# Kernel optimization log

Measured on AMD Instinct MI355X. Metric: run time of the kernel, lower is better.

## Reference

```python
import jax, jax.numpy as jnp
from jax import lax
import numpy as np
import math

B, N, A = 4096, 8, 5
IN_CH, HW = 3, 5
POS = 2
OBS_IN = POS + N            # 10
OBS_ACT_IN = OBS_IN + A     # 15
D = 128                     # obs_output_dim == d_k == embed width
STATE_DIM = 32 + OBS_IN     # 42
SAP_IN = 32 + OBS_ACT_IN    # 47


def setup_inputs() -> dict:
    key = jax.random.key(0)
    ks = jax.random.split(key, 24)
    w = lambda k, shape: (jax.random.normal(k, shape) * 0.05).astype(jnp.float32)
    return {
        "agent_states": jax.random.normal(ks[0], (B, N, IN_CH, HW, HW), jnp.float32),
        "agent_global_positions": jax.random.normal(ks[1], (B, N, POS), jnp.float32),
        "agent_one_hot_encoding": jax.random.uniform(ks[2], (B, N, N), jnp.float32),
        "policies": jax.random.uniform(ks[3], (B, N, A), jnp.float32),
        "actions": jax.random.uniform(ks[4], (B, N, A), jnp.float32),
        "conv1_w": w(ks[5], (16, IN_CH, 3, 3)), "conv1_b": w(ks[6], (16,)),
        "conv2_w": w(ks[7], (32, 16, 3, 3)),    "conv2_b": w(ks[8], (32,)),
        "se_w": w(ks[9], (STATE_DIM, 128)),     "se_b": w(ks[10], (128,)),
        "key_w": w(ks[11], (128, D)),           "key_b": w(ks[12], (D,)),
        "query_w": w(ks[13], (128, D)),         "query_b": w(ks[14], (D,)),
        "sap_w": w(ks[15], (SAP_IN, 128)),      "sap_b": w(ks[16], (128,)),
        "av_w": w(ks[17], (128, 128)),          "av_b": w(ks[18], (128,)),
        "f1_w": w(ks[19], (128, 64)),           "f1_b": w(ks[20], (64,)),
        "f2_w": w(ks[21], (64, 1)),             "f2_b": w(ks[22], (1,)),
    }


def _conv(x, w, b):
    y = lax.conv_general_dilated(x, w, (1, 1), 'VALID',
                                 dimension_numbers=('NCHW', 'OIHW', 'NCHW'))
    return y + b[None, :, None, None]


def reference(agent_states, agent_global_positions, agent_one_hot_encoding,
              policies, actions,
              conv1_w, conv1_b, conv2_w, conv2_b,
              se_w, se_b, key_w, key_b, query_w, query_b,
              sap_w, sap_b, av_w, av_b, f1_w, f1_b, f2_w, f2_b):
    leaky = lambda x: jnp.where(x >= 0, x, 0.01 * x)
    b, n = agent_states.shape[0], agent_states.shape[1]

    # CNN encoder: [B*N,3,5,5] -> [B*N,32,1,1]
    x = agent_states.reshape(b * n, IN_CH, HW, HW)
    h = leaky(_conv(x, conv1_w, conv1_b))
    h = leaky(_conv(h, conv2_w, conv2_b))
    pose_id = jnp.concatenate([agent_global_positions, agent_one_hot_encoding], axis=-1)
    states = jnp.concatenate([h.reshape(b, n, -1), pose_id], axis=-1)  # [B,N,42]

    states_embed = jnp.tanh(states @ se_w + se_b)                      # [B,N,128]
    k = states_embed @ key_w + key_b
    q = states_embed @ query_w + query_b
    weight = jax.nn.softmax(jnp.einsum('bqd,bkd->bqk', q, k) / math.sqrt(D), axis=-1)

    obs_actions = jnp.concatenate([states, actions], axis=-1)          # [B,N,47]
    obs_policy = jnp.concatenate([states, policies], axis=-1)         # [B,N,47]
    # place_policies puts the policy vector on the diagonal (i==j), action elsewhere.
    eye = jnp.eye(n, dtype=states.dtype)[None, :, :, None]             # [1,N,N,1]
    oap = eye * obs_policy[:, None, :, :] + (1.0 - eye) * obs_actions[:, None, :, :]  # [B,i,j,47]

    oap_embed = jnp.tanh(oap @ sap_w + sap_b)                          # [B,N,N,128]
    attn_vals = jnp.tanh(oap_embed @ av_w + av_b)                      # [B,i,j,128]

    # node_features[b,a,i,d] = sum_j weight[b,a,j] * attn_vals[b,i,j,d]
    # (replaces the original repeat -> broadcast-multiply -> sum over O(N^4) tensor)
    node_features = jnp.einsum('baj,bijd->baid', weight, attn_vals)    # [B,N,N,128]

    v = jnp.tanh(node_features @ f1_w + f1_b)
    value = v @ f2_w + f2_b                                            # [B,N,N,1]
    return value, weight
```

## Files before the change

### kernel.cpp

```cpp
#include <hip/hip_runtime.h>
#include <math.h>

#define NB 4096
#define NA 8
#define BN (NB*NA)

#define OFF_SE   0
#define OFF_SAP  4096
#define OFF_AV   8192
#define OFF_F1   16384
#define OFF_M    20480
#define OFF_U    28672
#define OFF_W2P  28800

typedef short short8 __attribute__((ext_vector_type(8)));
typedef float f32x4 __attribute__((ext_vector_type(4)));

#define MFMA(a,b,c) __builtin_amdgcn_mfma_f32_16x16x32_bf16(a,b,c,0,0,0)

__device__ __forceinline__ float fast_tanh(float x){
    float e = __expf(2.0f*x);
    return 1.0f - 2.0f*__builtin_amdgcn_rcpf(e+1.0f);
}
__device__ __forceinline__ unsigned bfr(float x){
    unsigned u = __float_as_uint(x);
    return (u + 0x7fffu + ((u>>16)&1u)) >> 16;
}
__device__ __forceinline__ unsigned pk2(float lo, float hi){
    return bfr(lo) | (bfr(hi)<<16);
}
__device__ __forceinline__ float bf2f(unsigned short s){
    return __uint_as_float(((unsigned)s)<<16);
}
__device__ __forceinline__ short8 fragld(const unsigned* p){
    union { uint4 u; short8 s; } cv;
    cv.u = *(const uint4*)p;
    return cv.s;
}

__global__ __launch_bounds__(256) void kW(const float* __restrict__ se_w,
        const float* __restrict__ sap_w, const float* __restrict__ av_w,
        const float* __restrict__ f1_w, const float* __restrict__ qw,
        const float* __restrict__ kw, const float* __restrict__ qb,
        const float* __restrict__ w2,
        unsigned* __restrict__ ws){
    int idx = blockIdx.x*256 + threadIdx.x;
    if (idx < 4096){
        int w = idx, tile = w>>9, rem = w&511;
        int ft = rem>>6, r2 = (rem>>2)&15, wi = rem&3;
        int f2 = tile*16 + r2, f1 = ft*8 + wi*2;
        float lo = (f1   < 42)? se_w[f1*128+f2]     : 0.f;
        float hi = (f1+1 < 42)? se_w[(f1+1)*128+f2] : 0.f;
        ws[OFF_SE + w] = pk2(lo,hi);
    } else if (idx < 8192){
        int w = idx-4096, tile = w>>9, rem = w&511;
        int ft = rem>>6, r2 = (rem>>2)&15, wi = rem&3;
        int f2 = tile*16 + r2, f1 = ft*8 + wi*2;
        float lo = (f1   < 47)? sap_w[f1*128+f2]     : 0.f;
        float hi = (f1+1 < 47)? sap_w[(f1+1)*128+f2] : 0.f;
        ws[OFF_SAP + w] = pk2(lo,hi);
    } else if (idx < 16384){
        int w = idx-8192, tile = w>>10, rem = w&1023;
        int ft = rem>>6, r2 = (rem>>2)&15, wi = rem&3;
        int f2 = tile*16 + r2, f1 = ft*8 + wi*2;
        ws[OFF_AV + w] = pk2(av_w[f1*128+f2], av_w[(f1+1)*128+f2]);
    } else if (idx < 20480){
        int w = idx-16384, tile = w>>10, rem = w&1023;
        int ft = rem>>6, r2 = (rem>>2)&15, wi = rem&3;
        int f2 = tile*16 + r2, f1 = ft*8 + wi*2;
        ws[OFF_F1 + w] = pk2(f1_w[f1*64+f2], f1_w[(f1+1)*64+f2]);
    } else if (idx < 28672){
        int w = idx-20480, tile = w>>10, rem = w&1023;
        int ft = rem>>6, r2 = (rem>>2)&15, wi = rem&3;
        int f2 = tile*16 + r2, e0 = ft*8 + wi*2;
        float lo=0.f, hi=0.f;
        for (int d=0; d<128; ++d){
            float kv = kw[f2*128+d];
            lo += qw[e0*128+d]*kv;
            hi += qw[(e0+1)*128+d]*kv;
        }
        ws[OFF_M + w] = pk2(lo,hi);
    } else if (idx < 28800){
        int f = idx-28672;
        float a = 0.f;
        for (int d=0; d<128; ++d) a += qb[d]*kw[f*128+d];
        ((float*)ws)[OFF_U + f] = a;
    } else if (idx < 31360){
        int w = idx-28800;
        int ftile = w/1280, rem = w - ftile*1280;
        int ft = rem>>6, r2 = (rem>>2)&15, wi = rem&3;
        int f = ftile*16 + r2, k0 = ft*8 + wi*2;
        float lo = (k0   < 144)? w2[f*144+k0]   : 0.f;
        float hi = (k0+1 < 144)? w2[f*144+k0+1] : 0.f;
        ws[OFF_W2P + w] = pk2(lo,hi);
    }
}

__global__ __launch_bounds__(256,2) void kF(const unsigned* __restrict__ ws,
        const float* __restrict__ xin, const float* __restrict__ pos,
        const float* __restrict__ oneh, const float* __restrict__ acts,
        const float* __restrict__ pols,
        const float* __restrict__ w1, const float* __restrict__ b1,
        const float* __restrict__ b2,
        const float* __restrict__ se_b,
        const float* __restrict__ sap_b, const float* __restrict__ av_b,
        const float* __restrict__ f1_b, const float* __restrict__ f2_w,
        const float* __restrict__ f2_b,
        float* __restrict__ wout, float* __restrict__ value){
    __shared__ unsigned SM[9216];
    __shared__ unsigned stPk[4096];
    __shared__ unsigned sA64[2304];
    __shared__ unsigned sP64[2304];
    __shared__ float s_w[512];
    __shared__ float s_bias[384];
    __shared__ float s_ub[256];
    const int t = threadIdx.x;
    const int wv = t>>6, lane = t&63;
    const int g = lane>>4, c = lane&15;

    float* c_in   = (float*)SM;
    unsigned* hpk = SM + 1216;
    float* c_ap   = (float*)(SM+6336);
    float* c_pose = (float*)(SM+6496);
    float* c_w1   = (float*)(SM+6656);
    float* c_b1   = (float*)(SM+7088);
    float* c_b2   = (float*)(SM+7104);
    for (int q=t; q<432; q+=256) c_w1[q] = w1[q];
    if (t<16) c_b1[t] = b1[t];
    if (t<32) c_b2[t] = b2[t];
    for (int q=t; q<512; q+=256) hpk[(q>>7)*1280 + 1152 + (q&127)] = 0;
    for (int q=t; q<384; q+=256)
        s_bias[q] = (q<128)? sap_b[q] : (q<256)? av_b[q-128] : (q<320)? f1_b[q-256] : f2_w[q-320];
    s_ub[t] = (t<128)? ((const float*)ws)[OFF_U+t] : se_b[t-128];

    for (int p=0; p<4; ++p){
        const size_t a0g = (size_t)blockIdx.x*64 + p*16;
        for (int q=t; q<1200; q+=256){
            int ag=q/75, r=q-ag*75;
            c_in[ag*76+r] = xin[a0g*75+q];
        }
        for (int q=t; q<160; q+=256){
            int ag=q/10, k=q-ag*10;
            c_ap[q]   = (k<5)? acts[(a0g+ag)*5+k] : pols[(a0g+ag)*5+(k-5)];
            c_pose[q] = (k<2)? pos[(a0g+ag)*2+k]  : oneh[(a0g+ag)*8+(k-2)];
        }
        __syncthreads();
        {
            const int ag = t&15, oc = t>>4;
            float w[27];
            #pragma unroll
            for (int i=0;i<27;++i) w[i]=c_w1[oc*27+i];
            float out[9];
            float bb = c_b1[oc];
            #pragma unroll
            for (int q=0;q<9;++q) out[q]=bb;
            #pragma unroll
            for (int ic=0;ic<3;++ic){
                float pin[25];
                #pragma unroll
                for (int i=0;i<25;++i) pin[i]=c_in[ag*76+ic*25+i];
                #pragma unroll
                for (int y=0;y<3;++y)
                  #pragma unroll
                  for (int x=0;x<3;++x)
                    #pragma unroll
                    for (int ky=0;ky<3;++ky)
                      #pragma unroll
                      for (int kx=0;kx<3;++kx)
                        out[y*3+x] += pin[(y+ky)*5+(x+kx)] * w[ic*9+ky*3+kx];
            }
            unsigned short* hp16 = (unsigned short*)(hpk + p*1280);
            #pragma unroll
            for (int q=0;q<9;++q){
                float v = out[q];
                v = (v>=0.f)? v : 0.01f*v;
                int k = oc*9+q;
                int word = (k>>3)*64 + ag*4 + ((k>>1)&3);
                hp16[word*2 + (k&1)] = (unsigned short)bfr(v);
            }
        }
        {
            const int ft4 = t>>6, r = (t>>2)&15, wi = t&3;
            const int f0 = 32 + ft4*8 + wi*2;
            float a0=0.f,a1=0.f,p0=0.f,p1=0.f;
            if (f0 < 42){ a0 = c_pose[r*10 + f0-32]; p0 = a0; }
            else if (f0 < 47){ a0 = c_ap[r*10 + f0-42]; p0 = c_ap[r*10+5 + f0-42]; }
            if (f0+1 < 42){ a1 = c_pose[r*10 + f0-31]; p1 = a1; }
            else if (f0+1 < 47){ a1 = c_ap[r*10 + f0-41]; p1 = c_ap[r*10+5 + f0-41]; }
            int word = p*512 + (4+ft4)*64 + r*4 + wi;
            stPk[word]      = pk2(a0,a1);
            stPk[2048+word] = pk2(p0,p1);
        }
        __syncthreads();
    }
    {
        const unsigned* hw = hpk + wv*1280;
        f32x4 c2[2];
        c2[0] = (f32x4){0.f,0.f,0.f,0.f};
        c2[1] = (f32x4){0.f,0.f,0.f,0.f};
        #pragma unroll
        for (int kt=0; kt<5; ++kt){
            short8 hb  = fragld(hw + kt*256 + lane*4);
            short8 w0f = fragld(ws + OFF_W2P + kt*256 + lane*4);
            short8 w1f = fragld(ws + OFF_W2P + 1280 + kt*256 + lane*4);
            c2[0] = MFMA(w0f, hb, c2[0]);
            c2[1] = MFMA(w1f, hb, c2[1]);
        }
        #pragma unroll
        for (int ft=0; ft<2; ++ft){
            const float* bp = &c_b2[ft*16 + g*4];
            float d0 = c2[ft][0]+bp[0]; d0 = (d0>=0.f)? d0 : 0.01f*d0;
            float d1 = c2[ft][1]+bp[1]; d1 = (d1>=0.f)? d1 : 0.01f*d1;
            float d2 = c2[ft][2]+bp[2]; d2 = (d2>=0.f)? d2 : 0.01f*d2;
            float d3 = c2[ft][3]+bp[3]; d3 = (d3>=0.f)? d3 : 0.01f*d3;
            int word = wv*512 + (2*ft + (g>>1))*64 + c*4 + (g&1)*2;
            uint2 pw = make_uint2(pk2(d0,d1), pk2(d2,d3));
            *(uint2*)&stPk[word] = pw;
            *(uint2*)&stPk[2048+word] = pw;
        }
    }
    __syncthreads();

    const int tile = blockIdx.x*4 + wv;
    short8 bfA0 = fragld(&stPk[wv*512 + lane*4]);
    short8 bfA1 = fragld(&stPk[wv*512 + 256 + lane*4]);
    short8 bfP0 = fragld(&stPk[2048 + wv*512 + lane*4]);
    short8 bfP1 = fragld(&stPk[2048 + wv*512 + 256 + lane*4]);
    unsigned (*s_stage)[2048] = (unsigned (*)[2048])&SM[0];
    unsigned* U1 = &SM[4096];
    unsigned* wS = &U1[wv*1280];
    unsigned* tS = &U1[wv*1280 + 1024];

    uint4 r0, r1;
#define PREF(off) { r0 = *(const uint4*)(ws + (off) + t*4); \
                    r1 = *(const uint4*)(ws + (off) + 1024 + t*4); }
#define WR(b) { *(uint4*)&s_stage[b][t*4] = r0; *(uint4*)&s_stage[b][1024 + t*4] = r1; }

    PREF(OFF_SE); WR(0);
    __syncthreads();

    f32x4 acc[8];
    #pragma unroll
    for (int i=0;i<8;++i) acc[i] = (f32x4){0.f,0.f,0.f,0.f};
    PREF(OFF_SE + 2048);
    #pragma unroll
    for (int ft=0; ft<4; ++ft){
        short8 a0 = fragld(&s_stage[0][ft*512 + lane*4]);
        short8 a1 = fragld(&s_stage[0][ft*512 + 256 + lane*4]);
        acc[ft] = MFMA(a0, bfA0, acc[ft]);
        acc[ft] = MFMA(a1, bfA1, acc[ft]);
    }
    WR(1); __syncthreads();
    PREF(OFF_M);
    #pragma unroll
    for (int ft=4; ft<8; ++ft){
        short8 a0 = fragld(&s_stage[1][(ft-4)*512 + lane*4]);
        short8 a1 = fragld(&s_stage[1][(ft-4)*512 + 256 + lane*4]);
        acc[ft] = MFMA(a0, bfA0, acc[ft]);
        acc[ft] = MFMA(a1, bfA1, acc[ft]);
    }
    WR(0);
    #pragma unroll
    for (int ft=0; ft<8; ++ft){
        const float* bp = &s_ub[128 + ft*16 + g*4];
        float d0 = fast_tanh(acc[ft][0]+bp[0]);
        float d1 = fast_tanh(acc[ft][1]+bp[1]);
        float d2 = fast_tanh(acc[ft][2]+bp[2]);
        float d3 = fast_tanh(acc[ft][3]+bp[3]);
        int word = (2*ft + (g>>1))*64 + c*4 + (g&1)*2;
        *(uint2*)&wS[word] = make_uint2(pk2(d0,d1), pk2(d2,d3));
    }
    short8 ef[4];
    #pragma unroll
    for (int kt=0; kt<4; ++kt) ef[kt] = fragld(&wS[kt*256 + lane*4]);
    __syncthreads();

    f32x4 L = (f32x4){0.f,0.f,0.f,0.f};
    #pragma unroll
    for (int i=0; i<4; ++i){
        const int nextOff = (i<3)? (OFF_M + (i+1)*2048) : OFF_SAP;
        PREF(nextOff);
        f32x4 a2[2];
        a2[0] = (f32x4){0.f,0.f,0.f,0.f};
        a2[1] = (f32x4){0.f,0.f,0.f,0.f};
        #pragma unroll
        for (int ftl=0; ftl<2; ++ftl)
          #pragma unroll
          for (int kt=0; kt<4; ++kt){
            short8 mf = fragld(&s_stage[i&1][ftl*1024 + kt*256 + lane*4]);
            a2[ftl] = MFMA(mf, ef[kt], a2[ftl]);
          }
        WR((i+1)&1);
        #pragma unroll
        for (int ftl=0; ftl<2; ++ftl){
            const float* up = &s_ub[(2*i+ftl)*16 + g*4];
            int word = (2*ftl + (g>>1))*64 + c*4 + (g&1)*2;
            *(uint2*)&tS[word] = make_uint2(pk2(a2[ftl][0]+up[0], a2[ftl][1]+up[1]),
                                            pk2(a2[ftl][2]+up[2], a2[ftl][3]+up[3]));
        }
        short8 tf = fragld(&tS[lane*4]);
        L = MFMA(tf, ef[i], L);
        __syncthreads();
    }
    {
        float sc[4];
        #pragma unroll
        for (int q=0;q<4;++q) sc[q] = L[q]*0.08838834764831845f;
        #pragma unroll
        for (int q=0;q<4;++q){
            float m = sc[q];
            m = fmaxf(m, __shfl_xor(m,1));
            m = fmaxf(m, __shfl_xor(m,2));
            m = fmaxf(m, __shfl_xor(m,4));
            float ex = __expf(sc[q]-m);
            float su = ex;
            su += __shfl_xor(su,1);
            su += __shfl_xor(su,2);
            su += __shfl_xor(su,4);
            sc[q] = ex/su;
        }
        if ((c>>3) == (g>>1)){
            int lb = wv*2 + (g>>1);
            int batch = tile*2 + (g>>1);
            int idx = ((g&1)*4)*8 + (c&7);
            #pragma unroll
            for (int q=0;q<4;++q){
                float v = sc[q];
                wout[batch*64 + idx + q*8] = v;
                s_w[lb*64 + idx + q*8] = v;
            }
        }
    }

    f32x4 aS[2][8];
    #pragma unroll
    for (int v=0;v<2;++v)
      #pragma unroll
      for (int i=0;i<8;++i) aS[v][i] = (f32x4){0.f,0.f,0.f,0.f};
    PREF(OFF_SAP + 2048);
    #pragma unroll
    for (int ft=0; ft<4; ++ft){
        short8 a0 = fragld(&s_stage[0][ft*512 + lane*4]);
        short8 a1 = fragld(&s_stage[0][ft*512 + 256 + lane*4]);
        aS[0][ft] = MFMA(a0, bfA0, aS[0][ft]);
        aS[0][ft] = MFMA(a1, bfA1, aS[0][ft]);
        aS[1][ft] = MFMA(a0, bfP0, aS[1][ft]);
        aS[1][ft] = MFMA(a1, bfP1, aS[1][ft]);
    }
    WR(1); __syncthreads();
    PREF(OFF_AV);
    #pragma unroll
    for (int ft=4; ft<8; ++ft){
        short8 a0 = fragld(&s_stage[1][(ft-4)*512 + lane*4]);
        short8 a1 = fragld(&s_stage[1][(ft-4)*512 + 256 + lane*4]);
        aS[0][ft] = MFMA(a0, bfA0, aS[0][ft]);
        aS[0][ft] = MFMA(a1, bfA1, aS[0][ft]);
        aS[1][ft] = MFMA(a0, bfP0, aS[1][ft]);
        aS[1][ft] = MFMA(a1, bfP1, aS[1][ft]);
    }
    WR(0);
    short8 spA[4], spP[4];
    #pragma unroll
    for (int ft=0; ft<8; ++ft){
        const float* bp = &s_bias[ft*16 + g*4];
        float d0 = fast_tanh(aS[0][ft][0]+bp[0]);
        float d1 = fast_tanh(aS[0][ft][1]+bp[1]);
        float d2 = fast_tanh(aS[0][ft][2]+bp[2]);
        float d3 = fast_tanh(aS[0][ft][3]+bp[3]);
        int word = (2*ft + (g>>1))*64 + c*4 + (g&1)*2;
        *(uint2*)&wS[word] = make_uint2(pk2(d0,d1), pk2(d2,d3));
    }
    #pragma unroll
    for (int kt=0; kt<4; ++kt) spA[kt] = fragld(&wS[kt*256 + lane*4]);
    #pragma unroll
    for (int ft=0; ft<8; ++ft){
        const float* bp = &s_bias[ft*16 + g*4];
        float d0 = fast_tanh(aS[1][ft][0]+bp[0]);
        float d1 = fast_tanh(aS[1][ft][1]+bp[1]);
        float d2 = fast_tanh(aS[1][ft][2]+bp[2]);
        float d3 = fast_tanh(aS[1][ft][3]+bp[3]);
        int word = (2*ft + (g>>1))*64 + c*4 + (g&1)*2;
        *(uint2*)&wS[word] = make_uint2(pk2(d0,d1), pk2(d2,d3));
    }
    #pragma unroll
    for (int kt=0; kt<4; ++kt) spP[kt] = fragld(&wS[kt*256 + lane*4]);
    __syncthreads();

    f32x4 aV[2][8];
    #pragma unroll
    for (int v=0;v<2;++v)
      #pragma unroll
      for (int i=0;i<8;++i) aV[v][i] = (f32x4){0.f,0.f,0.f,0.f};
    short8 avA[4], avP[4];
    #pragma unroll
    for (int i=0; i<4; ++i){
        const int nextOff = (i<3)? (OFF_AV + (i+1)*2048) : OFF_F1;
        PREF(nextOff);
        #pragma unroll
        for (int ftl=0; ftl<2; ++ftl){
            const int ft = 2*i + ftl;
            #pragma unroll
            for (int kt=0; kt<4; ++kt){
                short8 af = fragld(&s_stage[i&1][ftl*1024 + kt*256 + lane*4]);
                aV[0][ft] = MFMA(af, spA[kt], aV[0][ft]);
                aV[1][ft] = MFMA(af, spP[kt], aV[1][ft]);
            }
        }
        WR((i+1)&1);
        if (i==3){
            #pragma unroll
            for (int ft=0; ft<8; ++ft){
                const float* bp = &s_bias[128 + ft*16 + g*4];
                float d0 = fast_tanh(aV[0][ft][0]+bp[0]);
                float d1 = fast_tanh(aV[0][ft][1]+bp[1]);
                float d2 = fast_tanh(aV[0][ft][2]+bp[2]);
                float d3 = fast_tanh(aV[0][ft][3]+bp[3]);
                int word = (2*ft + (g>>1))*64 + c*4 + (g&1)*2;
                *(uint2*)&wS[word] = make_uint2(pk2(d0,d1), pk2(d2,d3));
            }
            #pragma unroll
            for (int kt=0; kt<4; ++kt) avA[kt] = fragld(&wS[kt*256 + lane*4]);
            #pragma unroll
            for (int ft=0; ft<8; ++ft){
                const float* bp = &s_bias[128 + ft*16 + g*4];
                float d0 = fast_tanh(aV[1][ft][0]+bp[0]);
                float d1 = fast_tanh(aV[1][ft][1]+bp[1]);
                float d2 = fast_tanh(aV[1][ft][2]+bp[2]);
                float d3 = fast_tanh(aV[1][ft][3]+bp[3]);
                int word = (2*ft + (g>>1))*64 + c*4 + (g&1)*2;
                *(uint2*)&wS[word] = make_uint2(pk2(d0,d1), pk2(d2,d3));
            }
            #pragma unroll
            for (int kt=0; kt<4; ++kt) avP[kt] = fragld(&wS[kt*256 + lane*4]);
        }
        __syncthreads();
    }

    f32x4 aF[2][4];
    #pragma unroll
    for (int v=0;v<2;++v)
      #pragma unroll
      for (int i=0;i<4;++i) aF[v][i] = (f32x4){0.f,0.f,0.f,0.f};
    PREF(OFF_F1 + 2048);
    #pragma unroll
    for (int ftl=0; ftl<2; ++ftl)
      #pragma unroll
      for (int kt=0; kt<4; ++kt){
        short8 af = fragld(&s_stage[0][ftl*1024 + kt*256 + lane*4]);
        aF[0][ftl] = MFMA(af, avA[kt], aF[0][ftl]);
        aF[1][ftl] = MFMA(af, avP[kt], aF[1][ftl]);
      }
    WR(1); __syncthreads();
    #pragma unroll
    for (int ftl=0; ftl<2; ++ftl)
      #pragma unroll
      for (int kt=0; kt<4; ++kt){
        short8 af = fragld(&s_stage[1][ftl*1024 + kt*256 + lane*4]);
        aF[0][2+ftl] = MFMA(af, avA[kt], aF[0][2+ftl]);
        aF[1][2+ftl] = MFMA(af, avP[kt], aF[1][2+ftl]);
      }
    {
        int row = wv*16 + c;
        #pragma unroll
        for (int v=0;v<2;++v){
            unsigned* dst = v? sP64 : sA64;
            #pragma unroll
            for (int ft=0; ft<4; ++ft){
                int idx = row*36 + ft*8 + 2*g;
                *(uint2*)&dst[idx] = make_uint2(pk2(aF[v][ft][0], aF[v][ft][1]),
                                                pk2(aF[v][ft][2], aF[v][ft][3]));
            }
        }
    }
    __syncthreads();
    float* s_b64 = (float*)U1;
    {
        const int bqa = t>>2, ccg = t&3;
        const int bq = bqa>>3, a = bqa&7;
        const float* wp = &s_w[bq*64 + a*8];
        f32x4 av0 = (f32x4){0.f,0.f,0.f,0.f};
        f32x4 av1 = (f32x4){0.f,0.f,0.f,0.f};
        f32x4 av2 = (f32x4){0.f,0.f,0.f,0.f};
        f32x4 av3 = (f32x4){0.f,0.f,0.f,0.f};
        #pragma unroll
        for (int j=0;j<8;++j){
            float wj = wp[j];
            const unsigned* rp = &sA64[(bq*8+j)*36 + ccg*8];
            short8 v0 = fragld(rp);
            short8 v1 = fragld(rp+4);
            av0[0] += wj*bf2f((unsigned short)v0[0]); av0[1] += wj*bf2f((unsigned short)v0[1]);
            av0[2] += wj*bf2f((unsigned short)v0[2]); av0[3] += wj*bf2f((unsigned short)v0[3]);
            av1[0] += wj*bf2f((unsigned short)v0[4]); av1[1] += wj*bf2f((unsigned short)v0[5]);
            av1[2] += wj*bf2f((unsigned short)v0[6]); av1[3] += wj*bf2f((unsigned short)v0[7]);
            av2[0] += wj*bf2f((unsigned short)v1[0]); av2[1] += wj*bf2f((unsigned short)v1[1]);
            av2[2] += wj*bf2f((unsigned short)v1[2]); av2[3] += wj*bf2f((unsigned short)v1[3]);
            av3[0] += wj*bf2f((unsigned short)v1[4]); av3[1] += wj*bf2f((unsigned short)v1[5]);
            av3[2] += wj*bf2f((unsigned short)v1[6]); av3[3] += wj*bf2f((unsigned short)v1[7]);
        }
        float* outp = &s_b64[bqa*68 + ccg*16];
        *(f32x4*)&outp[0]  = av0;
        *(f32x4*)&outp[4]  = av1;
        *(f32x4*)&outp[8]  = av2;
        *(f32x4*)&outp[12] = av3;
    }
    __syncthreads();
    #pragma unroll
    for (int k=0; k<2; ++k){
        int o = t + 256*k;
        int bq = o>>6, a = (o>>3)&7, i = o&7;
        float w_ai = s_w[bq*64 + a*8 + i];
        const float* pb = &s_b64[(bq*8+a)*68];
        const unsigned* pA = &sA64[(bq*8+i)*36];
        const unsigned* pP = &sP64[(bq*8+i)*36];
        float acc5 = 0.f;
        #pragma unroll
        for (int c8=0; c8<8; ++c8){
            f32x4 pb0 = *(const f32x4*)&pb[c8*8];
            f32x4 pb1 = *(const f32x4*)&pb[c8*8+4];
            short8 va = fragld(pA + c8*4);
            short8 vp = fragld(pP + c8*4);
            const float* fb = &s_bias[256 + c8*8];
            const float* fw = &s_bias[320 + c8*8];
            #pragma unroll
            for (int e=0;e<4;++e){
                float dd = bf2f((unsigned short)vp[e]) - bf2f((unsigned short)va[e]);
                acc5 += fast_tanh(pb0[e] + w_ai*dd + fb[e]) * fw[e];
            }
            #pragma unroll
            for (int e=0;e<4;++e){
                float dd = bf2f((unsigned short)vp[4+e]) - bf2f((unsigned short)va[4+e]);
                acc5 += fast_tanh(pb1[e] + w_ai*dd + fb[4+e]) * fw[4+e];
            }
        }
        value[(size_t)blockIdx.x*512 + o] = acc5 + f2_b[0];
    }
#undef PREF
#undef WR
}

extern "C" void kernel_launch(void* const* d_in, const int* in_sizes, int n_in,
                              void* d_out, int out_size, void* d_ws, size_t ws_size,
                              hipStream_t stream){
    const float* agent_states = (const float*)d_in[0];
    const float* pos    = (const float*)d_in[1];
    const float* oneh   = (const float*)d_in[2];
    const float* pols   = (const float*)d_in[3];
    const float* acts   = (const float*)d_in[4];
    const float* w1     = (const float*)d_in[5];
    const float* b1     = (const float*)d_in[6];
    const float* w2     = (const float*)d_in[7];
    const float* b2     = (const float*)d_in[8];
    const float* se_w   = (const float*)d_in[9];
    const float* se_b   = (const float*)d_in[10];
    const float* key_w  = (const float*)d_in[11];
    const float* query_w= (const float*)d_in[13];
    const float* query_b= (const float*)d_in[14];
    const float* sap_w  = (const float*)d_in[15];
    const float* sap_b  = (const float*)d_in[16];
    const float* av_w   = (const float*)d_in[17];
    const float* av_b   = (const float*)d_in[18];
    const float* f1_w   = (const float*)d_in[19];
    const float* f1_b   = (const float*)d_in[20];
    const float* f2_w   = (const float*)d_in[21];
    const float* f2_b   = (const float*)d_in[22];

    unsigned* ws = (unsigned*)d_ws;

    float* value = (float*)d_out;
    float* wout  = value + (size_t)NB*NA*NA;

    kW<<<123, 256, 0, stream>>>(se_w, sap_w, av_w, f1_w, query_w, key_w, query_b, w2, ws);
    kF<<<BN/64, 256, 0, stream>>>(ws, agent_states, pos, oneh, acts, pols,
                                  w1, b1, b2, se_b, sap_b, av_b, f1_b, f2_w, f2_b,
                                  wout, value);
}
```

Baseline: 51.52 us.

## Give each wave its own agent group for conv1 and drop block-wide barriers

The old code ran four passes, one per 16-agent group. Each pass staged inputs in shared memory, ran conv1 with all 256 threads, and needed two __syncthreads. Now each wave owns one 16-agent group, reads the conv input rows and the pose/action/policy features straight from global memory, and writes its own conv1 output and state tiles. Only an LDS waitcnt and a sched barrier remain before the conv2 MFMA. This removes most block barriers and the LDS staging, at the cost of uncoalesced per-lane global reads (75-float rows per lane) and more register pressure, since each lane holds two 9-output accumulators.

New measurement: 51.91 us. About the same (+0.8%).

```diff
diff --git a/kernel.cpp b/kernel.cpp
--- a/kernel.cpp
+++ b/kernel.cpp
@@ -118,89 +118,94 @@
     const int wv = t>>6, lane = t&63;
     const int g = lane>>4, c = lane&15;
 
-    float* c_in   = (float*)SM;
-    unsigned* hpk = SM + 1216;
-    float* c_ap   = (float*)(SM+6336);
-    float* c_pose = (float*)(SM+6496);
-    float* c_w1   = (float*)(SM+6656);
-    float* c_b1   = (float*)(SM+7088);
-    float* c_b2   = (float*)(SM+7104);
+    float* c_w1 = (float*)(SM+5120);
+    float* c_b1 = (float*)(SM+5552);
+    float* c_b2 = (float*)(SM+5568);
     for (int q=t; q<432; q+=256) c_w1[q] = w1[q];
     if (t<16) c_b1[t] = b1[t];
     if (t<32) c_b2[t] = b2[t];
-    for (int q=t; q<512; q+=256) hpk[(q>>7)*1280 + 1152 + (q&127)] = 0;
     for (int q=t; q<384; q+=256)
         s_bias[q] = (q<128)? sap_b[q] : (q<256)? av_b[q-128] : (q<320)? f1_b[q-256] : f2_w[q-320];
     s_ub[t] = (t<128)? ((const float*)ws)[OFF_U+t] : se_b[t-128];
-
-    for (int p=0; p<4; ++p){
-        const size_t a0g = (size_t)blockIdx.x*64 + p*16;
-        for (int q=t; q<1200; q+=256){
-            int ag=q/75, r=q-ag*75;
-            c_in[ag*76+r] = xin[a0g*75+q];
-        }
-        for (int q=t; q<160; q+=256){
-            int ag=q/10, k=q-ag*10;
-            c_ap[q]   = (k<5)? acts[(a0g+ag)*5+k] : pols[(a0g+ag)*5+(k-5)];
-            c_pose[q] = (k<2)? pos[(a0g+ag)*2+k]  : oneh[(a0g+ag)*8+(k-2)];
-        }
-        __syncthreads();
-        {
-            const int ag = t&15, oc = t>>4;
-            float w[27];
-            #pragma unroll
-            for (int i=0;i<27;++i) w[i]=c_w1[oc*27+i];
-            float out[9];
-            float bb = c_b1[oc];
-            #pragma unroll
-            for (int q=0;q<9;++q) out[q]=bb;
+    __syncthreads();
+
+    {
+        unsigned* hpk = SM + wv*1280;
+        unsigned short* hp16 = (unsigned short*)hpk;
+        const int ag = lane&15, ocb = lane>>4;
+        const size_t a0g = (size_t)blockIdx.x*64 + wv*16;
+        hpk[1152+lane] = 0;
+        hpk[1216+lane] = 0;
+        const float* xrow = xin + (a0g+ag)*75;
+        #pragma unroll
+        for (int half=0; half<2; ++half){
+            float out[2][9];
+            #pragma unroll
+            for (int j=0;j<2;++j){
+                float bb = c_b1[ocb + (half*2+j)*4];
+                #pragma unroll
+                for (int p=0;p<9;++p) out[j][p]=bb;
+            }
             #pragma unroll
             for (int ic=0;ic<3;++ic){
                 float pin[25];
                 #pragma unroll
-                for (int i=0;i<25;++i) pin[i]=c_in[ag*76+ic*25+i];
+                for (int i=0;i<25;++i) pin[i] = xrow[ic*25+i];
                 #pragma unroll
-                for (int y=0;y<3;++y)
-                  #pragma unroll
-                  for (int x=0;x<3;++x)
+                for (int j=0;j<2;++j){
+                    const float* wp = &c_w1[(ocb+(half*2+j)*4)*27 + ic*9];
+                    float w9[9];
                     #pragma unroll
-                    for (int ky=0;ky<3;++ky)
+                    for (int i=0;i<9;++i) w9[i]=wp[i];
+                    #pragma unroll
+                    for (int y=0;y<3;++y)
                       #pragma unroll
-                      for (int kx=0;kx<3;++kx)
-                        out[y*3+x] += pin[(y+ky)*5+(x+kx)] * w[ic*9+ky*3+kx];
-            }
-            unsigned short* hp16 = (unsigned short*)(hpk + p*1280);
-            #pragma unroll
-            for (int q=0;q<9;++q){
-                float v = out[q];
-                v = (v>=0.f)? v : 0.01f*v;
-                int k = oc*9+q;
-                int word = (k>>3)*64 + ag*4 + ((k>>1)&3);
-                hp16[word*2 + (k&1)] = (unsigned short)bfr(v);
+                      for (int x=0;x<3;++x)
+                        #pragma unroll
+                        for (int ky=0;ky<3;++ky)
+                          #pragma unroll
+                          for (int kx=0;kx<3;++kx)
+                            out[j][y*3+x] += pin[(y+ky)*5+(x+kx)] * w9[ky*3+kx];
+                }
+            }
+            #pragma unroll
+            for (int j=0;j<2;++j){
+                const int oc = ocb + (half*2+j)*4;
+                #pragma unroll
+                for (int p=0;p<9;++p){
+                    float v = out[j][p];
+                    v = (v>=0.f)? v : 0.01f*v;
+                    int k = oc*9+p;
+                    int word = (k>>3)*64 + ag*4 + ((k>>1)&3);
+                    hp16[word*2 + (k&1)] = (unsigned short)bfr(v);
+                }
             }
         }
         {
-            const int ft4 = t>>6, r = (t>>2)&15, wi = t&3;
-            const int f0 = 32 + ft4*8 + wi*2;
-            float a0=0.f,a1=0.f,p0=0.f,p1=0.f;
-            if (f0 < 42){ a0 = c_pose[r*10 + f0-32]; p0 = a0; }
-            else if (f0 < 47){ a0 = c_ap[r*10 + f0-42]; p0 = c_ap[r*10+5 + f0-42]; }
-            if (f0+1 < 42){ a1 = c_pose[r*10 + f0-31]; p1 = a1; }
-            else if (f0+1 < 47){ a1 = c_ap[r*10 + f0-41]; p1 = c_ap[r*10+5 + f0-41]; }
-            int word = p*512 + (4+ft4)*64 + r*4 + wi;
-            stPk[word]      = pk2(a0,a1);
-            stPk[2048+word] = pk2(p0,p1);
-        }
-        __syncthreads();
-    }
-    {
-        const unsigned* hw = hpk + wv*1280;
+            const int r = lane&15, ft4 = lane>>4;
+            const size_t row = a0g + r;
+            #pragma unroll
+            for (int wi=0; wi<4; ++wi){
+                int f0 = 32 + ft4*8 + wi*2;
+                float a0=0.f,a1=0.f,p0=0.f,p1=0.f;
+                if (f0 < 42){ float v = (f0<34)? pos[row*2+(f0-32)] : oneh[row*8+(f0-34)]; a0=v; p0=v; }
+                else if (f0 < 47){ a0 = acts[row*5+(f0-42)]; p0 = pols[row*5+(f0-42)]; }
+                int f1i = f0+1;
+                if (f1i < 42){ float v = (f1i<34)? pos[row*2+(f1i-32)] : oneh[row*8+(f1i-34)]; a1=v; p1=v; }
+                else if (f1i < 47){ a1 = acts[row*5+(f1i-42)]; p1 = pols[row*5+(f1i-42)]; }
+                int word = wv*512 + (4+ft4)*64 + r*4 + wi;
+                stPk[word]      = pk2(a0,a1);
+                stPk[2048+word] = pk2(p0,p1);
+            }
+        }
+        asm volatile("s_waitcnt lgkmcnt(0)" ::: "memory");
+        __builtin_amdgcn_sched_barrier(0);
         f32x4 c2[2];
         c2[0] = (f32x4){0.f,0.f,0.f,0.f};
         c2[1] = (f32x4){0.f,0.f,0.f,0.f};
         #pragma unroll
         for (int kt=0; kt<5; ++kt){
-            short8 hb  = fragld(hw + kt*256 + lane*4);
+            short8 hb  = fragld(hpk + kt*256 + lane*4);
             short8 w0f = fragld(ws + OFF_W2P + kt*256 + lane*4);
             short8 w1f = fragld(ws + OFF_W2P + 1280 + kt*256 + lane*4);
             c2[0] = MFMA(w0f, hb, c2[0]);
```
